# Kernel optimization log

Measured on AMD Instinct MI355X. Metric: run time of the kernel, lower is better.

Reference implementation:

```python
import jax, jax.numpy as jnp
import numpy as np

B, T, D, H = 8, 1024, 1024, 16

def setup_inputs() -> dict:
    key = jax.random.key(0)
    k1, k2, k3, k4, k5 = jax.random.split(key, 5)
    x = jax.random.normal(k1, (B, T, D), dtype=jnp.float32)
    mask = jnp.tril(jnp.ones((T, T), dtype=bool))[None, None]  # [1,1,T,T] causal
    s = 0.02
    W_attn = jax.random.normal(k2, (D, 3 * D), dtype=jnp.float32) * s
    b_attn = jnp.zeros((3 * D,), dtype=jnp.float32)
    W_proj = jax.random.normal(k3, (D, D), dtype=jnp.float32) * s
    b_proj = jnp.zeros((D,), dtype=jnp.float32)
    return {"x": x, "mask": mask, "W_attn": W_attn, "b_attn": b_attn,
            "W_proj": W_proj, "b_proj": b_proj}

def reference(x, mask, W_attn, b_attn, W_proj, b_proj):
    num_heads = H
    b, t, d = x.shape
    hd = d // num_heads
    qkv = x @ W_attn + b_attn                      # [b,t,3d]
    q, k, v = jnp.split(qkv, 3, axis=-1)
    def to_heads(a):
        return a.reshape(b, t, num_heads, hd).transpose(0, 2, 1, 3)  # [b,h,t,hd]
    q, k, v = to_heads(q), to_heads(k), to_heads(v)
    scale = 1.0 / jnp.sqrt(jnp.float32(hd))
    attn = jnp.einsum('bhqd,bhkd->bhqk', q, k) * scale
    attn = jnp.where(mask, attn, jnp.finfo(jnp.float32).min)
    attn = jax.nn.softmax(attn, axis=-1)
    o = jnp.einsum('bhqk,bhkd->bhqd', attn, v)
    o = o.transpose(0, 2, 1, 3).reshape(b, t, d)   # [b,t,d]
    return o @ W_proj + b_proj
```

## Files before the change

### kernel.cpp

```cpp
#include <hip/hip_runtime.h>
#include <cstdint>


typedef __attribute__((ext_vector_type(8))) short bf16x8;
typedef __attribute__((ext_vector_type(4))) float f32x4;

__device__ __forceinline__ short f2b(float x) {
  unsigned u = __builtin_bit_cast(unsigned, x);
  u += 0x7fffu + ((u >> 16) & 1u);
  return (short)(u >> 16);
}

__device__ __forceinline__ unsigned cvtpk(float lo, float hi) {
  unsigned d;
  asm("v_cvt_pk_bf16_f32 %0, %1, %2" : "=v"(d) : "v"(lo), "v"(hi));
  return d;
}

__device__ __forceinline__ void gl2lds16(short* l, const short* g) {
  __builtin_amdgcn_global_load_lds(
      (const __attribute__((address_space(1))) void*)g,
      (__attribute__((address_space(3))) void*)l, 16, 0, 0);
}


__global__ void prep_fused(const float* __restrict__ x, short* __restrict__ xb,
                           const float* __restrict__ Wa, short* __restrict__ WaT,
                           const float* __restrict__ Wp, short* __restrict__ WpT) {
  __shared__ float tile[32][33];
  const int bid = blockIdx.x;
  const int t = threadIdx.x;
  if (bid < 2048) {
    int base = bid * 256 + t;
#pragma unroll
    for (int it = 0; it < 4; ++it) {
      int i = base + it * 524288;
      float4 v = ((const float4*)x)[i];
      short4 o;
      o.x = f2b(v.x); o.y = f2b(v.y); o.z = f2b(v.z); o.w = f2b(v.w);
      ((short4*)xb)[i] = o;
    }
    return;
  }
  const float* in;
  short* out;
  int C, bx, by;
  if (bid < 5120) {
    int id = bid - 2048;
    in = Wa; out = WaT; C = 3072; bx = id % 96; by = id / 96;
  } else {
    int id = bid - 5120;
    in = Wp; out = WpT; C = 1024; bx = id % 32; by = id / 32;
  }
  int c0 = bx * 32, r0 = by * 32;
  int tx = t & 31, ty = t >> 5;
#pragma unroll
  for (int i = 0; i < 32; i += 8)
    tile[ty + i][tx] = in[(long)(r0 + ty + i) * C + c0 + tx];
  __syncthreads();
  int oc = t >> 3, g = t & 7;
  short4 v;
  v.x = f2b(tile[g * 4 + 0][oc]);
  v.y = f2b(tile[g * 4 + 1][oc]);
  v.z = f2b(tile[g * 4 + 2][oc]);
  v.w = f2b(tile[g * 4 + 3][oc]);
  *(short4*)(out + (long)(c0 + oc) * 1024 + r0 + g * 4) = v;
}


template <int EPI>
__global__ __launch_bounds__(256, 4) void gemm_bt(
    const short* __restrict__ A, const short* __restrict__ Bt,
    const float* __restrict__ bias, float* __restrict__ outF,
    short* __restrict__ qh, short* __restrict__ kh, short* __restrict__ vT,
    int M, int N, int K) {
  __shared__ short At[128 * 64];
  __shared__ short Bl[128 * 64];
  const int t = threadIdx.x;
  const int wave = t >> 6, lane = t & 63;
  const int quad = lane >> 4, l15 = lane & 15;
  const int wr = wave >> 1, wc = wave & 1;
  const int m0 = blockIdx.y * 128, n0 = blockIdx.x * 128;

  f32x4 acc[4][4] = {};

  const int srow = t >> 3;
  const int sch0 = t & 7;

  for (int k0 = 0; k0 < K; k0 += 64) {
    __syncthreads();
#pragma unroll
    for (int c = 0; c < 4; ++c) {
      int row = c * 32 + srow;
      int ch = sch0 ^ (row & 7);
      gl2lds16(At + (c * 256 + t) * 8, A + (long)(m0 + row) * K + k0 + ch * 8);
      gl2lds16(Bl + (c * 256 + t) * 8, Bt + (long)(n0 + row) * K + k0 + ch * 8);
    }
    asm volatile("s_waitcnt vmcnt(0)" ::: "memory");
    __syncthreads();

#pragma unroll
    for (int s = 0; s < 2; ++s) {
      const int cx = (s * 4 + quad) ^ (l15 & 7);
      bf16x8 af[4], bfr[4];
#pragma unroll
      for (int i = 0; i < 4; ++i)
        af[i] = *(const bf16x8*)(At + (wr * 64 + i * 16 + l15) * 64 + cx * 8);
#pragma unroll
      for (int j = 0; j < 4; ++j)
        bfr[j] = *(const bf16x8*)(Bl + (wc * 64 + j * 16 + l15) * 64 + cx * 8);
#pragma unroll
      for (int i = 0; i < 4; ++i)
#pragma unroll
        for (int j = 0; j < 4; ++j)
          acc[i][j] = __builtin_amdgcn_mfma_f32_16x16x32_bf16(af[i], bfr[j],
                                                              acc[i][j], 0, 0, 0);
    }
  }

  if (EPI == 1) {
#pragma unroll
    for (int j = 0; j < 4; ++j) {
      int col = n0 + wc * 64 + j * 16 + l15;
      float bv = bias[col];
#pragma unroll
      for (int i = 0; i < 4; ++i)
#pragma unroll
        for (int r = 0; r < 4; ++r) {
          int row = m0 + wr * 64 + i * 16 + quad * 4 + r;
          outF[(long)row * N + col] = acc[i][j][r] + bv;
        }
    }
  } else {
    const int sec = n0 >> 10;
    const int b = m0 >> 10;
    const float sc = (sec == 0) ? (0.125f * 1.44269504089f) : 1.0f;
#pragma unroll
    for (int j = 0; j < 4; ++j) {
      int col = n0 + wc * 64 + j * 16 + l15;
      float bv = bias[col];
      int d = col & 1023, h = d >> 6, dh = d & 63;
      if (sec == 2) {
        long base = ((long)(b * 16 + h) * 64 + dh) * 1024;
#pragma unroll
        for (int i = 0; i < 4; ++i) {
          int tt0 = (m0 & 1023) + wr * 64 + (i >> 1) * 32 + quad * 8 + (i & 1) * 4;
          short4 v;
          v.x = f2b(acc[i][j][0] + bv);
          v.y = f2b(acc[i][j][1] + bv);
          v.z = f2b(acc[i][j][2] + bv);
          v.w = f2b(acc[i][j][3] + bv);
          *(short4*)(vT + base + tt0) = v;
        }
      } else {
        short* dst = (sec == 0) ? qh : kh;
        long hbase = ((long)(b * 16 + h) * 1024) * 64 + dh;
#pragma unroll
        for (int i = 0; i < 4; ++i)
#pragma unroll
          for (int r = 0; r < 4; ++r) {
            int tt = (m0 & 1023) + wr * 64 + i * 16 + quad * 4 + r;
            dst[hbase + (long)tt * 64] = f2b((acc[i][j][r] + bv) * sc);
          }
      }
    }
  }
}


__global__ __launch_bounds__(256, 2) void attn_kernel(
    const short* __restrict__ qh, const short* __restrict__ kh,
    const short* __restrict__ vT, short* __restrict__ attout) {
  __shared__ short Kb[4][64 * 64];
  __shared__ short Vb[4][64 * 64];
  __shared__ short P_lds[4][16][64];
  const int bh = blockIdx.x;
  const int p = blockIdx.y;
  const int t = threadIdx.x;
  const int wave = t >> 6, lane = t & 63, quad = lane >> 4, l15 = lane & 15;
  const short* q_head = qh + (long)bh * 1024 * 64;
  const short* k_head = kh + (long)bh * 1024 * 64;
  const short* v_head = vT + (long)bh * 64 * 1024;
  const int b_ = bh >> 4, h_ = bh & 15;

  const int qt[4] = {p, 7 - p, 8 + p, 15 - p};

  auto stage = [&](int kt) {
    const int buf = kt & 3;
    const int kk0 = kt * 64;
#pragma unroll
    for (int i = 0; i < 2; ++i) {
      int s = i * 256 + t;
      int row = s >> 3, cg = (s & 7) ^ (row & 7);
      gl2lds16(&Kb[buf][s * 8], k_head + (kk0 + row) * 64 + cg * 8);
    }
#pragma unroll
    for (int i = 0; i < 2; ++i) {
      int s = i * 256 + t;
      int row = s >> 3, cg = (s & 7) ^ (row & 7);
      gl2lds16(&Vb[buf][s * 8], v_head + row * 1024 + kk0 + cg * 8);
    }
  };

  bf16x8 qf[4][2];
#pragma unroll
  for (int i = 0; i < 4; ++i) {
    int qb = qt[i] * 64 + wave * 16;
#pragma unroll
    for (int s = 0; s < 2; ++s)
      qf[i][s] = *(const bf16x8*)(q_head + (qb + l15) * 64 + s * 32 + quad * 8);
  }

  float l[4] = {};
  f32x4 o[4][4] = {};

  const int nkt = qt[3] + 1;

  stage(0);
  if (1 < nkt) stage(1);
  __syncthreads();

  auto computeTile = [&](int kt) {
    const int buf = kt & 3;
    const short* Kt = Kb[buf];
    const short* Vt = Vb[buf];

    bf16x8 kfr[4][2], vfr[4][2];
#pragma unroll
    for (int jj = 0; jj < 4; ++jj) {
      int row = jj * 16 + l15;
#pragma unroll
      for (int s = 0; s < 2; ++s) {
        int off = ((s * 4 + quad) ^ (row & 7)) * 8;
        kfr[jj][s] = *(const bf16x8*)(Kt + row * 64 + off);
        vfr[jj][s] = *(const bf16x8*)(Vt + row * 64 + off);
      }
    }

#pragma unroll
    for (int i = 0; i < 4; ++i) {
      if (kt <= qt[i]) {
        f32x4 s4[4] = {};
#pragma unroll
        for (int jj = 0; jj < 4; ++jj) {
          s4[jj] = __builtin_amdgcn_mfma_f32_16x16x32_bf16(kfr[jj][0], qf[i][0],
                                                           s4[jj], 0, 0, 0);
          s4[jj] = __builtin_amdgcn_mfma_f32_16x16x32_bf16(kfr[jj][1], qf[i][1],
                                                           s4[jj], 0, 0, 0);
        }
        float ev[4][4];
        float ls = 0.f;
        if (kt == qt[i]) {
          const int qg = qt[i] * 64 + wave * 16 + l15;
#pragma unroll
          for (int jj = 0; jj < 4; ++jj) {
            const int kb = kt * 64 + jj * 16 + quad * 4;
#pragma unroll
            for (int r = 0; r < 4; ++r) {
              float e = __builtin_amdgcn_exp2f(s4[jj][r]);
              if (kb + r > qg) e = 0.f;
              ev[jj][r] = e;
              ls += e;
            }
          }
        } else {
#pragma unroll
          for (int jj = 0; jj < 4; ++jj)
#pragma unroll
            for (int r = 0; r < 4; ++r) {
              float e = __builtin_amdgcn_exp2f(s4[jj][r]);
              ev[jj][r] = e;
              ls += e;
            }
        }
        l[i] += ls;
        int4 pd0, pd1;
        pd0.x = (int)cvtpk(ev[0][0], ev[0][1]);
        pd0.y = (int)cvtpk(ev[0][2], ev[0][3]);
        pd0.z = (int)cvtpk(ev[1][0], ev[1][1]);
        pd0.w = (int)cvtpk(ev[1][2], ev[1][3]);
        pd1.x = (int)cvtpk(ev[2][0], ev[2][1]);
        pd1.y = (int)cvtpk(ev[2][2], ev[2][3]);
        pd1.z = (int)cvtpk(ev[3][0], ev[3][1]);
        pd1.w = (int)cvtpk(ev[3][2], ev[3][3]);
        bf16x8 pf0 = __builtin_bit_cast(bf16x8, pd0);
        bf16x8 pf1 = __builtin_bit_cast(bf16x8, pd1);
#pragma unroll
        for (int dj = 0; dj < 4; ++dj) {
          o[i][dj] = __builtin_amdgcn_mfma_f32_16x16x32_bf16(pf0, vfr[dj][0],
                                                             o[i][dj], 0, 0, 0);
          o[i][dj] = __builtin_amdgcn_mfma_f32_16x16x32_bf16(pf1, vfr[dj][1],
                                                             o[i][dj], 0, 0, 0);
        }
      }
    }
  };

#pragma unroll 1
  for (int kt2 = 0; kt2 < nkt; kt2 += 2) {
    if (kt2 + 2 < nkt) stage(kt2 + 2);
    if (kt2 + 3 < nkt) stage(kt2 + 3);
    computeTile(kt2);
    if (kt2 + 1 < nkt) computeTile(kt2 + 1);
    __syncthreads();
  }

#pragma unroll
  for (int i = 0; i < 4; ++i) {
    l[i] += __shfl_xor(l[i], 16);
    l[i] += __shfl_xor(l[i], 32);
  }

  const int erow = lane >> 3, ech = lane & 7;
#pragma unroll
  for (int i = 0; i < 4; ++i) {
    float inv[4];
#pragma unroll
    for (int r = 0; r < 4; ++r) {
      float lr = __shfl(l[i], quad * 4 + r);
      inv[r] = __builtin_amdgcn_rcpf(lr);
    }
    const int qb = qt[i] * 64 + wave * 16;
#pragma unroll
    for (int dj = 0; dj < 4; ++dj) {
      int ch = dj * 2 + (l15 >> 3), co = l15 & 7;
#pragma unroll
      for (int r = 0; r < 4; ++r) {
        int row = quad * 4 + r;
        P_lds[wave][row][(ch ^ (row & 7)) * 8 + co] = f2b(o[i][dj][r] * inv[r]);
      }
    }
    asm volatile("s_waitcnt lgkmcnt(0)" ::: "memory");
#pragma unroll
    for (int pass = 0; pass < 2; ++pass) {
      int row = pass * 8 + erow;
      bf16x8 v = *(const bf16x8*)(&P_lds[wave][row][(ech ^ (row & 7)) * 8]);
      long g = (long)b_ * 1024 + qb + row;
      *(bf16x8*)(attout + g * 1024 + h_ * 64 + ech * 8) = v;
    }
    asm volatile("s_waitcnt lgkmcnt(0)" ::: "memory");
  }
}


extern "C" void kernel_launch(void* const* d_in, const int* in_sizes, int n_in,
                              void* d_out, int out_size, void* d_ws,
                              size_t ws_size, hipStream_t stream) {
  const float* x = (const float*)d_in[0];
  const float* W_attn = (const float*)d_in[2];
  const float* b_attn = (const float*)d_in[3];
  const float* W_proj = (const float*)d_in[4];
  const float* b_proj = (const float*)d_in[5];
  float* out = (float*)d_out;

  char* ws = (char*)d_ws;
  const size_t MB = 1u << 20;
  short* xb = (short*)(ws);
  short* WaT = (short*)(ws + 16 * MB);
  short* WpT = (short*)(ws + 22 * MB);
  short* qh = (short*)(ws + 24 * MB);
  short* kh = (short*)(ws + 40 * MB);
  short* vT = (short*)(ws + 56 * MB);
  short* attout = xb;

  prep_fused<<<6144, 256, 0, stream>>>(x, xb, W_attn, WaT, W_proj, WpT);
  gemm_bt<0><<<dim3(3072 / 128, 8192 / 128), 256, 0, stream>>>(
      xb, WaT, b_attn, nullptr, qh, kh, vT, 8192, 3072, 1024);
  attn_kernel<<<dim3(128, 4), 256, 0, stream>>>(qh, kh, vT, attout);
  gemm_bt<1><<<dim3(1024 / 128, 8192 / 128), 256, 0, stream>>>(
      attout, WpT, b_proj, out, nullptr, nullptr, nullptr, 8192, 1024, 1024);
}
```

Before: 203.2 us.

## Batch QK and PV MFMAs across query subtiles with priority hints

Restructures the attention tile compute into three phases: all QK^T MFMAs for the four query subtiles, then exp/mask/pack for all of them, then all PV MFMAs. Each phase's MFMAs are wrapped in s_setprio so matrix-core work is issued back to back and overlaps with other waves' exp work. It also lowers the GEMM kernel's launch_bounds occupancy hint from 4 to 3 blocks to give it more registers. The batched layout keeps 16 score vectors and 8 packed P fragments live at once, which raises register pressure in the attention kernel and may cost occupancy or cause spills.

```diff
diff --git a/kernel.cpp b/kernel.cpp
--- a/kernel.cpp
+++ b/kernel.cpp
@@ -69,7 +69,7 @@
 
 
 template <int EPI>
-__global__ __launch_bounds__(256, 4) void gemm_bt(
+__global__ __launch_bounds__(256, 3) void gemm_bt(
     const short* __restrict__ A, const short* __restrict__ Bt,
     const float* __restrict__ bias, float* __restrict__ outF,
     short* __restrict__ qh, short* __restrict__ kh, short* __restrict__ vT,
@@ -237,17 +237,27 @@
       }
     }
 
+    f32x4 s4[4][4];
+    __builtin_amdgcn_s_setprio(1);
 #pragma unroll
     for (int i = 0; i < 4; ++i) {
       if (kt <= qt[i]) {
-        f32x4 s4[4] = {};
 #pragma unroll
         for (int jj = 0; jj < 4; ++jj) {
-          s4[jj] = __builtin_amdgcn_mfma_f32_16x16x32_bf16(kfr[jj][0], qf[i][0],
-                                                           s4[jj], 0, 0, 0);
-          s4[jj] = __builtin_amdgcn_mfma_f32_16x16x32_bf16(kfr[jj][1], qf[i][1],
-                                                           s4[jj], 0, 0, 0);
-        }
+          f32x4 z = {};
+          z = __builtin_amdgcn_mfma_f32_16x16x32_bf16(kfr[jj][0], qf[i][0], z,
+                                                      0, 0, 0);
+          s4[i][jj] = __builtin_amdgcn_mfma_f32_16x16x32_bf16(
+              kfr[jj][1], qf[i][1], z, 0, 0, 0);
+        }
+      }
+    }
+    __builtin_amdgcn_s_setprio(0);
+
+    bf16x8 pf[4][2];
+#pragma unroll
+    for (int i = 0; i < 4; ++i) {
+      if (kt <= qt[i]) {
         float ev[4][4];
         float ls = 0.f;
         if (kt == qt[i]) {
@@ -257,7 +267,7 @@
             const int kb = kt * 64 + jj * 16 + quad * 4;
 #pragma unroll
             for (int r = 0; r < 4; ++r) {
-              float e = __builtin_amdgcn_exp2f(s4[jj][r]);
+              float e = __builtin_amdgcn_exp2f(s4[i][jj][r]);
               if (kb + r > qg) e = 0.f;
               ev[jj][r] = e;
               ls += e;
@@ -268,7 +278,7 @@
           for (int jj = 0; jj < 4; ++jj)
 #pragma unroll
             for (int r = 0; r < 4; ++r) {
-              float e = __builtin_amdgcn_exp2f(s4[jj][r]);
+              float e = __builtin_amdgcn_exp2f(s4[i][jj][r]);
               ev[jj][r] = e;
               ls += e;
             }
@@ -283,17 +293,25 @@
         pd1.y = (int)cvtpk(ev[2][2], ev[2][3]);
         pd1.z = (int)cvtpk(ev[3][0], ev[3][1]);
         pd1.w = (int)cvtpk(ev[3][2], ev[3][3]);
-        bf16x8 pf0 = __builtin_bit_cast(bf16x8, pd0);
-        bf16x8 pf1 = __builtin_bit_cast(bf16x8, pd1);
+        pf[i][0] = __builtin_bit_cast(bf16x8, pd0);
+        pf[i][1] = __builtin_bit_cast(bf16x8, pd1);
+      }
+    }
+
+    __builtin_amdgcn_s_setprio(1);
+#pragma unroll
+    for (int i = 0; i < 4; ++i) {
+      if (kt <= qt[i]) {
 #pragma unroll
         for (int dj = 0; dj < 4; ++dj) {
-          o[i][dj] = __builtin_amdgcn_mfma_f32_16x16x32_bf16(pf0, vfr[dj][0],
-                                                             o[i][dj], 0, 0, 0);
-          o[i][dj] = __builtin_amdgcn_mfma_f32_16x16x32_bf16(pf1, vfr[dj][1],
-                                                             o[i][dj], 0, 0, 0);
-        }
-      }
-    }
+          o[i][dj] = __builtin_amdgcn_mfma_f32_16x16x32_bf16(
+              pf[i][0], vfr[dj][0], o[i][dj], 0, 0, 0);
+          o[i][dj] = __builtin_amdgcn_mfma_f32_16x16x32_bf16(
+              pf[i][1], vfr[dj][1], o[i][dj], 0, 0, 0);
+        }
+      }
+    }
+    __builtin_amdgcn_s_setprio(0);
   };
 
 #pragma unroll 1
```

Measured after the change: 216.4 us. 1.06x slower.
